# Performance work log

Measured on AMD Instinct MI355X. Metric: run time of the kernel, lower is better.

The kernel has to match this reference:

```python
import jax, jax.numpy as jnp
import numpy as np

B, S, D, H = 4, 2048, 512, 8
HD = D // H


def rotate_half(t):
    half = t.shape[-1] // 2
    return jnp.concatenate([-t[..., half:], t[..., :half]], axis=-1)


def setup_inputs() -> dict:
    key = jax.random.key(0)
    ks = jax.random.split(key, 8)
    x = jax.random.normal(ks[0], (B, S, D), dtype=jnp.float32)
    # realistic rotary tables built from angles
    inv_freq = 1.0 / (10000.0 ** (jnp.arange(0, D // 2, dtype=jnp.float32) / (D // 2)))
    ang = jnp.arange(S, dtype=jnp.float32)[:, None] * inv_freq[None, :]  # [S, D/2]
    ang = jnp.concatenate([ang, ang], axis=-1)  # [S, D]
    cos_emb = jnp.cos(ang)[None]  # [1, S, D]
    sin_emb = jnp.sin(ang)[None]
    mask = jax.random.randint(ks[1], (B, S, S), 0, 2).astype(jnp.bool_)
    scale = 1.0 / np.sqrt(D)
    wq = jax.random.normal(ks[2], (D, D), dtype=jnp.float32) * scale
    wk = jax.random.normal(ks[3], (D, D), dtype=jnp.float32) * scale
    wv = jax.random.normal(ks[4], (D, D), dtype=jnp.float32) * scale
    wo = jax.random.normal(ks[5], (D, D), dtype=jnp.float32) * scale
    return {"x": x, "cos_emb": cos_emb, "sin_emb": sin_emb, "mask": mask,
            "wq": wq, "wk": wk, "wv": wv, "wo": wo}


def reference(x, cos_emb, sin_emb, mask, wq, wk, wv, wo):
    bsz, seqlen, dim = x.shape
    # projections (weights stored as [in, out])
    xq = x @ wq
    xk = x @ wk
    xv = x @ wv
    # RoPE applied over full dim before head split (as in original)
    xq = xq * cos_emb + rotate_half(xq) * sin_emb
    xk = xk * cos_emb + rotate_half(xk) * sin_emb
    # split heads: [B, H, S, HD]
    xq = xq.reshape(bsz, seqlen, H, HD).transpose(0, 2, 1, 3)
    xk = xk.reshape(bsz, seqlen, H, HD).transpose(0, 2, 1, 3)
    xv = xv.reshape(bsz, seqlen, H, HD).transpose(0, 2, 1, 3)
    scores = jnp.einsum('bhqd,bhkd->bhqk', xq, xk) / jnp.sqrt(jnp.float32(HD))
    scores = scores + (~mask)[:, None].astype(scores.dtype) * (-1e9)
    scores = jax.nn.softmax(scores.astype(jnp.float32), axis=-1).astype(xq.dtype)
    scores = scores * mask[:, None].astype(scores.dtype)
    out = jnp.einsum('bhqk,bhkd->bhqd', scores, xv)
    out = out.transpose(0, 2, 1, 3).reshape(bsz, seqlen, dim)
    return out @ wo
```

## Files before the change

kernel.cpp:

```cpp
#include <hip/hip_runtime.h>
#include <hip/hip_bf16.h>

typedef __bf16 bf16x8 __attribute__((ext_vector_type(8)));
typedef float f32x4 __attribute__((ext_vector_type(4)));
typedef short short8 __attribute__((ext_vector_type(8)));

#define MFMA16(a, b, c) __builtin_amdgcn_mfma_f32_16x16x32_bf16((a), (b), (c), 0, 0, 0)

static constexpr int S = 2048;
static constexpr int D = 512;
static constexpr int HD = 64;
static constexpr int KBLK = 64;
#define QSCALE 0.18033688011112042f

typedef __attribute__((address_space(1))) const unsigned int gu32;
typedef __attribute__((address_space(3))) unsigned int lu32;

__device__ __forceinline__ void gll16(const void* g, void* l) {
  __builtin_amdgcn_global_load_lds((gu32*)g, (lu32*)l, 16, 0, 0);
}

__device__ __forceinline__ unsigned short f2b(float f) {
  return __builtin_bit_cast(unsigned short, __float2bfloat16(f));
}
__device__ __forceinline__ float b2f(unsigned short u) {
  return __builtin_bit_cast(float, (unsigned)u << 16);
}

__global__ void maskbits_kernel(const int* __restrict__ m, unsigned long long* __restrict__ bits) {
  int gid = blockIdx.x * 256 + threadIdx.x;
  int lane = threadIdx.x & 63;
  unsigned long long w = __ballot(m[gid] != 0);
  if (lane == 0) bits[gid >> 6] = w;
}

__global__ void cast_x_kernel(const float* __restrict__ x, unsigned short* __restrict__ xb) {
  int idx = blockIdx.x * 256 + threadIdx.x;
  float4 v = ((const float4*)x)[idx];
  ushort4 o;
  o.x = f2b(v.x); o.y = f2b(v.y); o.z = f2b(v.z); o.w = f2b(v.w);
  ((ushort4*)xb)[idx] = o;
}

__global__ void wtrans4_kernel(const float* __restrict__ wq, const float* __restrict__ wk,
                               const float* __restrict__ wv, const float* __restrict__ wo,
                               unsigned short* __restrict__ wqkvT, unsigned short* __restrict__ woT) {
  __shared__ float t[64][65];
  const int z = blockIdx.z;
  const float* w = (z == 0) ? wq : (z == 1) ? wk : (z == 2) ? wv : wo;
  unsigned short* dst = (z < 3) ? wqkvT + (size_t)z * 512 * 512 : woT;
  const int i0 = blockIdx.x * 64, o0 = blockIdx.y * 64;
  for (int it = 0; it < 16; ++it) {
    int idx = it * 256 + threadIdx.x;
    int ii = idx >> 6, oo = idx & 63;
    t[oo][ii] = w[(size_t)(i0 + ii) * 512 + o0 + oo];
  }
  __syncthreads();
  for (int it = 0; it < 16; ++it) {
    int idx = it * 256 + threadIdx.x;
    int oo = idx >> 6, ii = idx & 63;
    dst[(size_t)(o0 + oo) * 512 + i0 + ii] = f2b(t[oo][ii]);
  }
}

__global__ __launch_bounds__(256)
void gemm2(const unsigned short* __restrict__ A, const unsigned short* __restrict__ Bt,
           int M, int N, int K, float* __restrict__ Cf,
           unsigned short* __restrict__ qd, unsigned short* __restrict__ kd,
           unsigned short* __restrict__ vtd, int mode) {
  __shared__ alignas(16) unsigned short lds[2][2][4096];
  const int tid = threadIdx.x;
  const int lane = tid & 63, l15 = lane & 15, lg = lane >> 4;
  const int wave = tid >> 6;
  const int m0 = blockIdx.x * 128, n0 = blockIdx.y * 128;
  const int wm = (wave >> 1) * 64, wn = (wave & 1) * 64;
  const int wbase = wave * 512;
  const int grow = tid >> 2, gcol = (tid & 3) * 8;
  f32x4 acc[4][4] = {};
  const int nt = K / 32;

#define GSTAGE(sb, kk)                                                              \
  do {                                                                              \
    gll16(&A[(size_t)(m0 + grow) * K + (kk) + gcol], &lds[sb][0][wbase]);           \
    gll16(&A[(size_t)(m0 + 64 + grow) * K + (kk) + gcol], &lds[sb][0][2048 + wbase]);\
    gll16(&Bt[(size_t)(n0 + grow) * K + (kk) + gcol], &lds[sb][1][wbase]);          \
    gll16(&Bt[(size_t)(n0 + 64 + grow) * K + (kk) + gcol], &lds[sb][1][2048 + wbase]);\
  } while (0)

  GSTAGE(0, 0);
  asm volatile("s_waitcnt vmcnt(0)" ::: "memory");
  __syncthreads();
  for (int t = 0; t < nt; ++t) {
    const int cur = t & 1;
    if (t + 1 < nt) GSTAGE(cur ^ 1, (t + 1) * 32);
    bf16x8 af[4], bfr[4];
#pragma unroll
    for (int i = 0; i < 4; ++i) {
      af[i]  = *(const bf16x8*)&lds[cur][0][(wm + i * 16 + l15) * 32 + lg * 8];
      bfr[i] = *(const bf16x8*)&lds[cur][1][(wn + i * 16 + l15) * 32 + lg * 8];
    }
    __builtin_amdgcn_s_setprio(1);
#pragma unroll
    for (int i = 0; i < 4; ++i)
#pragma unroll
      for (int j = 0; j < 4; ++j)
        acc[i][j] = MFMA16(af[i], bfr[j], acc[i][j]);
    __builtin_amdgcn_s_setprio(0);
    asm volatile("s_waitcnt vmcnt(0)" ::: "memory");
    __syncthreads();
  }
#undef GSTAGE

  if (mode == 0) {
#pragma unroll
    for (int i = 0; i < 4; ++i)
#pragma unroll
      for (int j = 0; j < 4; ++j)
#pragma unroll
        for (int r = 0; r < 4; ++r)
          Cf[(size_t)(m0 + wm + i * 16 + lg * 4 + r) * N + (n0 + wn + j * 16 + l15)] = acc[i][j][r];
  } else {
    const int sel = n0 >> 9;
    const int nb = (n0 & 511) + wn;
    if (sel < 2) {
      unsigned short* dst = (sel == 0) ? qd : kd;
#pragma unroll
      for (int i = 0; i < 4; ++i)
#pragma unroll
        for (int j = 0; j < 4; ++j)
#pragma unroll
          for (int r = 0; r < 4; ++r) {
            const int m = m0 + wm + i * 16 + lg * 4 + r;
            const int nn = nb + j * 16 + l15;
            dst[(((size_t)(m >> 11) * 8 + (nn >> 6)) * 2048 + (m & 2047)) * 64 + (nn & 63)] =
                f2b(acc[i][j][r]);
          }
    } else {
#pragma unroll
      for (int i = 0; i < 4; ++i)
#pragma unroll
        for (int j = 0; j < 4; ++j)
#pragma unroll
          for (int r = 0; r < 4; ++r) {
            const int m = m0 + wm + i * 16 + lg * 4 + r;
            const int nn = nb + j * 16 + l15;
            vtd[(((size_t)(m >> 11) * 8 + (nn >> 6)) * 64 + (nn & 63)) * 2048 + (m & 2047)] =
                f2b(acc[i][j][r]);
          }
    }
  }
}

__global__ void rope_pair_kernel(const unsigned short* __restrict__ qpre, const unsigned short* __restrict__ kpre,
                                 const float* __restrict__ cose, const float* __restrict__ sine,
                                 unsigned short* __restrict__ qb, unsigned short* __restrict__ kb) {
  const int idx = blockIdx.x * 256 + threadIdx.x;
  const int hd0 = (idx & 7) * 8;
  const int rr = idx >> 3;
  const int b = rr >> 13, h = (rr >> 11) & 3, s = rr & 2047;
  const size_t lo = ((size_t)(b * 8 + h) * 2048 + s) * 64 + hd0;
  const size_t hi = lo + (size_t)4 * 2048 * 64;
  const int d0 = h * 64 + hd0;
  short8 qlo = *(const short8*)&qpre[lo];
  short8 qhi = *(const short8*)&qpre[hi];
  short8 klo = *(const short8*)&kpre[lo];
  short8 khi = *(const short8*)&kpre[hi];
  float4 c0 = *(const float4*)&cose[(size_t)s * 512 + d0];
  float4 c1 = *(const float4*)&cose[(size_t)s * 512 + d0 + 4];
  float4 s0 = *(const float4*)&sine[(size_t)s * 512 + d0];
  float4 s1 = *(const float4*)&sine[(size_t)s * 512 + d0 + 4];
  float cc[8] = {c0.x, c0.y, c0.z, c0.w, c1.x, c1.y, c1.z, c1.w};
  float ss[8] = {s0.x, s0.y, s0.z, s0.w, s1.x, s1.y, s1.z, s1.w};
  short8 qolo, qohi, kolo, kohi;
#pragma unroll
  for (int j = 0; j < 8; ++j) {
    float ql = b2f((unsigned short)qlo[j]), qh = b2f((unsigned short)qhi[j]);
    float kl = b2f((unsigned short)klo[j]), kh = b2f((unsigned short)khi[j]);
    qolo[j] = (short)f2b((ql * cc[j] - qh * ss[j]) * QSCALE);
    qohi[j] = (short)f2b((qh * cc[j] + ql * ss[j]) * QSCALE);
    kolo[j] = (short)f2b(kl * cc[j] - kh * ss[j]);
    kohi[j] = (short)f2b(kh * cc[j] + kl * ss[j]);
  }
  *(short8*)&qb[lo] = qolo;
  *(short8*)&qb[hi] = qohi;
  *(short8*)&kb[lo] = kolo;
  *(short8*)&kb[hi] = kohi;
}

__global__ __launch_bounds__(512)
void flash_kernel(const unsigned short* __restrict__ qb, const unsigned short* __restrict__ kb,
                  const unsigned short* __restrict__ vtb, const unsigned long long* __restrict__ mbits,
                  float* __restrict__ op0, float* __restrict__ op1,
                  float* __restrict__ ls0, float* __restrict__ ls1) {
  __shared__ alignas(16) unsigned short kv[3][2][4096];
  __shared__ alignas(16) f32x4 btab[16];
  const int tid = threadIdx.x;
  const int wave = tid >> 6, lane = tid & 63;
  const int l15 = lane & 15, lg = lane >> 4;
  const int swz = (l15 & 7) << 4;
  const int wgid = blockIdx.x;
  const int slot = wgid >> 3;
  const int bh = (wgid & 7) * 4 + (slot & 3);
  const int rest = slot >> 2;
  const int kh = rest & 1;
  const int q0 = (rest >> 1) * 128 + wave * 16;
  const int b = bh >> 3, h = bh & 7;
  const int kbase = kh * 1024;
  const unsigned short* Q = qb + ((size_t)bh * S + q0) * HD;
  const unsigned short* Kp = kb + (size_t)bh * S * HD;
  const unsigned short* Vt = vtb + (size_t)bh * HD * S;
  const unsigned long long* Mrow = mbits + ((size_t)b * S + q0 + l15) * (S / 64) + kh * 16;
  float* opart = kh ? op1 : op0;
  float* lsum = kh ? ls1 : ls0;

  const int srow = tid >> 3;
  const int scol = ((tid & 7) ^ (srow & 7)) * 8;
  const int ksrow = ((srow & 15) >> 2) * 8 + ((srow >> 4) & 1) * 4 + (srow & 3) + (srow >> 5) * 32;
  const int wbase = wave * 512;

  if (tid < 16) {
    f32x4 e;
    e[0] = (tid & 1) ? 0.f : -300.f;
    e[1] = (tid & 2) ? 0.f : -300.f;
    e[2] = (tid & 4) ? 0.f : -300.f;
    e[3] = (tid & 8) ? 0.f : -300.f;
    btab[tid] = e;
  }

  bf16x8 qf0 = *(const bf16x8*)&Q[l15 * HD + lg * 8];
  bf16x8 qf1 = *(const bf16x8*)&Q[l15 * HD + 32 + lg * 8];
  f32x4 o[4] = {};
  float lpart = 0.f;
  const int lgs8 = lg * 8;

  unsigned long long wA = Mrow[0];
  gll16(&Kp[(size_t)(kbase + ksrow) * HD + scol], &kv[0][0][wbase]);
  gll16(&Vt[(size_t)srow * S + kbase + scol], &kv[0][1][wbase]);
  unsigned long long wB = Mrow[1];
  gll16(&Kp[(size_t)(kbase + 64 + ksrow) * HD + scol], &kv[1][0][wbase]);
  gll16(&Vt[(size_t)srow * S + kbase + 64 + scol], &kv[1][1][wbase]);
  asm volatile("s_waitcnt vmcnt(3) lgkmcnt(0)" ::: "memory");
  __builtin_amdgcn_s_barrier();

  int bi = 0;
  for (int t = 0; t < 16; ++t) {
    unsigned long long wC = 0;
    if (t + 2 < 16) {
      const int kn = kbase + (t + 2) * KBLK;
      const int bn = (bi == 0) ? 2 : bi - 1;
      wC = Mrow[t + 2];
      gll16(&Kp[(size_t)(kn + ksrow) * HD + scol], &kv[bn][0][wbase]);
      gll16(&Vt[(size_t)srow * S + kn + scol], &kv[bn][1][wbase]);
    }
    const char* kbp = (const char*)&kv[bi][0][0];
    const char* vbp = (const char*)&kv[bi][1][0];

    f32x4 sc[4] = {};
    __builtin_amdgcn_s_setprio(1);
#pragma unroll
    for (int n = 0; n < 4; ++n) {
      const int cb = (n * 16 + l15) * 128 + ((lg * 16) ^ swz);
      bf16x8 kf0 = *(const bf16x8*)(kbp + cb);
      bf16x8 kf1 = *(const bf16x8*)(kbp + (cb ^ 64));
      sc[n] = MFMA16(kf0, qf0, sc[n]);
      sc[n] = MFMA16(kf1, qf1, sc[n]);
    }
    __builtin_amdgcn_s_setprio(0);

    f32x4 pv[4];
    {
      const unsigned nib0 = (unsigned)(wA >> (lgs8 + 0)) & 15u;
      const unsigned nib1 = (unsigned)(wA >> (lgs8 + 4)) & 15u;
      const unsigned nib2 = (unsigned)(wA >> (lgs8 + 32)) & 15u;
      const unsigned nib3 = (unsigned)(wA >> (lgs8 + 36)) & 15u;
      const f32x4 b0 = btab[nib0], b1 = btab[nib1], b2 = btab[nib2], b3 = btab[nib3];
#pragma unroll
      for (int r = 0; r < 4; ++r) {
        pv[0][r] = __builtin_amdgcn_exp2f(sc[0][r] + b0[r]);
        pv[1][r] = __builtin_amdgcn_exp2f(sc[1][r] + b1[r]);
        pv[2][r] = __builtin_amdgcn_exp2f(sc[2][r] + b2[r]);
        pv[3][r] = __builtin_amdgcn_exp2f(sc[3][r] + b3[r]);
      }
    }
    f32x4 s4 = (pv[0] + pv[1]) + (pv[2] + pv[3]);
    lpart += (s4[0] + s4[1]) + (s4[2] + s4[3]);

    bf16x8 pf0, pf1;
#pragma unroll
    for (int j = 0; j < 4; ++j) {
      pf0[j]     = (__bf16)pv[0][j];
      pf0[j + 4] = (__bf16)pv[1][j];
      pf1[j]     = (__bf16)pv[2][j];
      pf1[j + 4] = (__bf16)pv[3][j];
    }

    __builtin_amdgcn_s_setprio(1);
#pragma unroll
    for (int n = 0; n < 4; ++n) {
      const int cb = (n * 16 + l15) * 128 + ((lg * 16) ^ swz);
      bf16x8 vf0 = *(const bf16x8*)(vbp + cb);
      bf16x8 vf1 = *(const bf16x8*)(vbp + (cb ^ 64));
      o[n] = MFMA16(pf0, vf0, o[n]);
      o[n] = MFMA16(pf1, vf1, o[n]);
    }
    __builtin_amdgcn_s_setprio(0);

    if (t < 14) { asm volatile("s_waitcnt vmcnt(3)" ::: "memory"); }
    else        { asm volatile("s_waitcnt vmcnt(0)" ::: "memory"); }
    __builtin_amdgcn_s_barrier();
    wA = wB; wB = wC;
    bi = (bi == 2) ? 0 : bi + 1;
  }

  lpart += __shfl_xor(lpart, 16);
  lpart += __shfl_xor(lpart, 32);
  if (lg == 0) lsum[(size_t)bh * S + q0 + l15] = lpart;
#pragma unroll
  for (int r = 0; r < 4; ++r)
#pragma unroll
    for (int n = 0; n < 4; ++n)
      opart[((size_t)(b * S + q0 + lg * 4 + r)) * D + h * HD + n * 16 + l15] = o[n][r];
}

__global__ __launch_bounds__(256)
void gemm_fused(const float* __restrict__ op0, const float* __restrict__ op1,
                const float* __restrict__ ls0, const float* __restrict__ ls1,
                const unsigned short* __restrict__ Bt, float* __restrict__ C) {
  __shared__ alignas(16) unsigned short ldsA[2][2048];
  __shared__ alignas(16) unsigned short ldsB[2][4096];
  __shared__ float invt[512];
  const int tid = threadIdx.x;
  const int lane = tid & 63, l15 = lane & 15, lg = lane >> 4;
  const int wave = tid >> 6;
  const int m0 = blockIdx.x * 64, n0 = blockIdx.y * 128;
  const int wm = (wave >> 1) * 32, wn = (wave & 1) * 64;
  const int wbase = wave * 512;
  const int grow = tid >> 2, gcol = (tid & 3) * 8;
  const int arow = m0 + (tid >> 2);
  const size_t abase = (size_t)arow * 512 + (tid & 3) * 8;
  f32x4 acc[2][4] = {};

  for (int e = tid; e < 512; e += 256) {
    const int row = e >> 3, hh = e & 7;
    const int m = m0 + row;
    const size_t li = ((size_t)((m >> 11) * 8 + hh)) * 2048 + (m & 2047);
    const float l = ls0[li] + ls1[li];
    invt[e] = (l > 0.f) ? 1.f / l : 0.f;
  }

#define BSTAGE(sb, kk)                                                               \
  do {                                                                               \
    gll16(&Bt[(size_t)(n0 + grow) * 512 + (kk) + gcol], &ldsB[sb][wbase]);           \
    gll16(&Bt[(size_t)(n0 + 64 + grow) * 512 + (kk) + gcol], &ldsB[sb][2048 + wbase]);\
  } while (0)

  float4 a0, a1, p0, p1;
#define ALOAD(kk)                                          \
  do {                                                     \
    a0 = *(const float4*)&op0[abase + (kk)];               \
    a1 = *(const float4*)&op0[abase + (kk) + 4];           \
    p0 = *(const float4*)&op1[abase + (kk)];               \
    p1 = *(const float4*)&op1[abase + (kk) + 4];           \
  } while (0)

#define AWRITE(sb, kk)                                                       \
  do {                                                                       \
    const float inv = invt[((tid >> 2) << 3) | ((kk) >> 6)];                 \
    short8 pk;                                                               \
    pk[0] = (short)f2b((a0.x + p0.x) * inv);                                 \
    pk[1] = (short)f2b((a0.y + p0.y) * inv);                                 \
    pk[2] = (short)f2b((a0.z + p0.z) * inv);                                 \
    pk[3] = (short)f2b((a0.w + p0.w) * inv);                                 \
    pk[4] = (short)f2b((a1.x + p1.x) * inv);                                 \
    pk[5] = (short)f2b((a1.y + p1.y) * inv);                                 \
    pk[6] = (short)f2b((a1.z + p1.z) * inv);                                 \
    pk[7] = (short)f2b((a1.w + p1.w) * inv);                                 \
    *(short8*)&ldsA[sb][(tid >> 2) * 32 + (tid & 3) * 8] = pk;               \
  } while (0)

  ALOAD(0);
  BSTAGE(0, 0);
  __syncthreads();
  AWRITE(0, 0);
  __syncthreads();

  for (int t = 0; t < 16; ++t) {
    const int cur = t & 1;
    const bool have = (t + 1 < 16);
    if (have) { ALOAD((t + 1) * 32); BSTAGE(cur ^ 1, (t + 1) * 32); }
    bf16x8 af[2], bfr[4];
#pragma unroll
    for (int i = 0; i < 2; ++i)
      af[i] = *(const bf16x8*)&ldsA[cur][(wm + i * 16 + l15) * 32 + lg * 8];
#pragma unroll
    for (int j = 0; j < 4; ++j)
      bfr[j] = *(const bf16x8*)&ldsB[cur][(wn + j * 16 + l15) * 32 + lg * 8];
    __builtin_amdgcn_s_setprio(1);
#pragma unroll
    for (int i = 0; i < 2; ++i)
#pragma unroll
      for (int j = 0; j < 4; ++j)
        acc[i][j] = MFMA16(af[i], bfr[j], acc[i][j]);
    __builtin_amdgcn_s_setprio(0);
    asm volatile("s_waitcnt vmcnt(0)" ::: "memory");
    __syncthreads();
    if (have) AWRITE(cur ^ 1, (t + 1) * 32);
    __syncthreads();
  }
#undef BSTAGE
#undef ALOAD
#undef AWRITE

#pragma unroll
  for (int i = 0; i < 2; ++i)
#pragma unroll
    for (int j = 0; j < 4; ++j)
#pragma unroll
      for (int r = 0; r < 4; ++r)
        C[(size_t)(m0 + wm + i * 16 + lg * 4 + r) * 512 + (n0 + wn + j * 16 + l15)] = acc[i][j][r];
}

extern "C" void kernel_launch(void* const* d_in, const int* in_sizes, int n_in,
                              void* d_out, int out_size, void* d_ws, size_t ws_size,
                              hipStream_t stream) {
  const float* x = (const float*)d_in[0];
  const float* cose = (const float*)d_in[1];
  const float* sine = (const float*)d_in[2];
  const int* mask = (const int*)d_in[3];
  const float* wq = (const float*)d_in[4];
  const float* wk = (const float*)d_in[5];
  const float* wv = (const float*)d_in[6];
  const float* wo = (const float*)d_in[7];
  float* out = (float*)d_out;
  char* ws = (char*)d_ws;

  unsigned short* xb    = (unsigned short*)(ws);
  unsigned short* wqkvT = (unsigned short*)(ws + 8388608);
  unsigned short* woT   = (unsigned short*)(ws + 9961472);
  unsigned short* qpre  = (unsigned short*)(ws + 10485760);
  unsigned short* kpre  = (unsigned short*)(ws + 18874368);
  unsigned short* qbh   = (unsigned short*)(ws + 35651584);
  unsigned short* kbh   = (unsigned short*)(ws + 44040192);
  unsigned short* vtb   = (unsigned short*)(ws + 52428800);
  unsigned long long* mbits = (unsigned long long*)(ws + 60817408);
  float* op0 = (float*)(ws + 10485760);
  float* op1 = (float*)(ws + 62914560);
  float* ls0 = (float*)(ws + 79691776);
  float* ls1 = (float*)(ws + 79953920);

  maskbits_kernel<<<65536, 256, 0, stream>>>(mask, mbits);
  cast_x_kernel<<<4096, 256, 0, stream>>>(x, xb);
  wtrans4_kernel<<<dim3(8, 8, 4), 256, 0, stream>>>(wq, wk, wv, wo, wqkvT, woT);
  gemm2<<<dim3(64, 12), 256, 0, stream>>>(xb, wqkvT, 8192, 1536, 512, nullptr, qpre, kpre, vtb, 1);
  rope_pair_kernel<<<1024, 256, 0, stream>>>(qpre, kpre, cose, sine, qbh, kbh);
  flash_kernel<<<1024, 512, 0, stream>>>(qbh, kbh, vtb, mbits, op0, op1, ls0, ls1);
  gemm_fused<<<dim3(128, 4), 256, 0, stream>>>(op0, op1, ls0, ls1, woT, out);
}
```

Measured before the change: 131.7 us.

## Switch flash attention to 32x32 MFMA with 32-row waves and remap GEMM grids

The flash kernel now uses 32x32x16 bf16 MFMA. Each wave covers 32 query rows, the block drops to 256 threads, and the K/V LDS pipeline goes from triple to double buffering with a full wait each iteration. The mask-bit bias lookup and output writes are remapped to the 32x32 accumulator layout. Both GEMM kernels also switch to a 1D grid with grouped tile ordering (8 M-tiles per group) for better L2 reuse. The larger MFMA tiles are meant to cut LDS fragment reads per flop, at the cost of less prefetch depth and more registers per wave.

New measurement: 174.9 us. 32.8% more time.

```diff
diff --git a/kernel.cpp b/kernel.cpp
--- a/kernel.cpp
+++ b/kernel.cpp
@@ -3,9 +3,11 @@
 
 typedef __bf16 bf16x8 __attribute__((ext_vector_type(8)));
 typedef float f32x4 __attribute__((ext_vector_type(4)));
+typedef float f32x16 __attribute__((ext_vector_type(16)));
 typedef short short8 __attribute__((ext_vector_type(8)));
 
 #define MFMA16(a, b, c) __builtin_amdgcn_mfma_f32_16x16x32_bf16((a), (b), (c), 0, 0, 0)
+#define MFMA32(a, b, c) __builtin_amdgcn_mfma_f32_32x32x16_bf16((a), (b), (c), 0, 0, 0)
 
 static constexpr int S = 2048;
 static constexpr int D = 512;
@@ -67,12 +69,14 @@
 void gemm2(const unsigned short* __restrict__ A, const unsigned short* __restrict__ Bt,
            int M, int N, int K, float* __restrict__ Cf,
            unsigned short* __restrict__ qd, unsigned short* __restrict__ kd,
-           unsigned short* __restrict__ vtd, int mode) {
+           unsigned short* __restrict__ vtd, int mode, int nblk) {
   __shared__ alignas(16) unsigned short lds[2][2][4096];
   const int tid = threadIdx.x;
   const int lane = tid & 63, l15 = lane & 15, lg = lane >> 4;
   const int wave = tid >> 6;
-  const int m0 = blockIdx.x * 128, n0 = blockIdx.y * 128;
+  const int wgid = blockIdx.x;
+  const int xg = wgid & 7, tg = wgid >> 3;
+  const int m0 = ((tg / nblk) * 8 + xg) * 128, n0 = (tg % nblk) * 128;
   const int wm = (wave >> 1) * 64, wn = (wave & 1) * 64;
   const int wbase = wave * 512;
   const int grow = tid >> 2, gcol = (tid & 3) * 8;
@@ -187,35 +191,36 @@
   *(short8*)&kb[hi] = kohi;
 }
 
-__global__ __launch_bounds__(512)
+__global__ __launch_bounds__(256, 4)
 void flash_kernel(const unsigned short* __restrict__ qb, const unsigned short* __restrict__ kb,
                   const unsigned short* __restrict__ vtb, const unsigned long long* __restrict__ mbits,
                   float* __restrict__ op0, float* __restrict__ op1,
                   float* __restrict__ ls0, float* __restrict__ ls1) {
-  __shared__ alignas(16) unsigned short kv[3][2][4096];
+  __shared__ alignas(16) unsigned short kv[2][2][4096];
   __shared__ alignas(16) f32x4 btab[16];
   const int tid = threadIdx.x;
   const int wave = tid >> 6, lane = tid & 63;
-  const int l15 = lane & 15, lg = lane >> 4;
-  const int swz = (l15 & 7) << 4;
+  const int l31 = lane & 31, lh = lane >> 5;
+  const int swz7 = l31 & 7;
   const int wgid = blockIdx.x;
   const int slot = wgid >> 3;
   const int bh = (wgid & 7) * 4 + (slot & 3);
   const int rest = slot >> 2;
   const int kh = rest & 1;
-  const int q0 = (rest >> 1) * 128 + wave * 16;
+  const int q0 = (rest >> 1) * 128 + wave * 32;
   const int b = bh >> 3, h = bh & 7;
   const int kbase = kh * 1024;
   const unsigned short* Q = qb + ((size_t)bh * S + q0) * HD;
   const unsigned short* Kp = kb + (size_t)bh * S * HD;
   const unsigned short* Vt = vtb + (size_t)bh * HD * S;
-  const unsigned long long* Mrow = mbits + ((size_t)b * S + q0 + l15) * (S / 64) + kh * 16;
+  const unsigned long long* Mrow = mbits + ((size_t)b * S + q0 + l31) * (S / 64) + kh * 16;
   float* opart = kh ? op1 : op0;
   float* lsum = kh ? ls1 : ls0;
 
   const int srow = tid >> 3;
-  const int scol = ((tid & 7) ^ (srow & 7)) * 8;
-  const int ksrow = ((srow & 15) >> 2) * 8 + ((srow >> 4) & 1) * 4 + (srow & 3) + (srow >> 5) * 32;
+  const int ch = tid & 7;
+  const int scol = (ch ^ (srow & 7)) * 8;
+  const int pif = 16 * ((srow >> 4) & 1) + 8 * ((srow >> 2) & 1) + 4 * ((srow >> 3) & 1) + (srow & 3);
   const int wbase = wave * 512;
 
   if (tid < 16) {
@@ -227,99 +232,106 @@
     btab[tid] = e;
   }
 
-  bf16x8 qf0 = *(const bf16x8*)&Q[l15 * HD + lg * 8];
-  bf16x8 qf1 = *(const bf16x8*)&Q[l15 * HD + 32 + lg * 8];
-  f32x4 o[4] = {};
+  bf16x8 qf[4];
+#pragma unroll
+  for (int wp = 0; wp < 4; ++wp)
+    qf[wp] = *(const bf16x8*)&Q[l31 * HD + wp * 16 + 8 * lh];
+  f32x16 o0 = {}, o1 = {};
   float lpart = 0.f;
-  const int lgs8 = lg * 8;
+  const int mb = lh * 8;
+
+#define FSTAGE(sb, kn)                                                               \
+  do {                                                                               \
+    gll16(&Kp[(size_t)((kn) + pif) * HD + scol], &kv[sb][0][wbase]);                 \
+    gll16(&Kp[(size_t)((kn) + 32 + pif) * HD + scol], &kv[sb][0][2048 + wbase]);     \
+    gll16(&Vt[(size_t)srow * S + (kn) + scol], &kv[sb][1][wbase]);                   \
+    gll16(&Vt[(size_t)(srow + 32) * S + (kn) + scol], &kv[sb][1][2048 + wbase]);     \
+  } while (0)
 
   unsigned long long wA = Mrow[0];
-  gll16(&Kp[(size_t)(kbase + ksrow) * HD + scol], &kv[0][0][wbase]);
-  gll16(&Vt[(size_t)srow * S + kbase + scol], &kv[0][1][wbase]);
-  unsigned long long wB = Mrow[1];
-  gll16(&Kp[(size_t)(kbase + 64 + ksrow) * HD + scol], &kv[1][0][wbase]);
-  gll16(&Vt[(size_t)srow * S + kbase + 64 + scol], &kv[1][1][wbase]);
-  asm volatile("s_waitcnt vmcnt(3) lgkmcnt(0)" ::: "memory");
-  __builtin_amdgcn_s_barrier();
-
-  int bi = 0;
+  FSTAGE(0, kbase);
+  asm volatile("s_waitcnt vmcnt(0) lgkmcnt(0)" ::: "memory");
+  __syncthreads();
+
   for (int t = 0; t < 16; ++t) {
-    unsigned long long wC = 0;
-    if (t + 2 < 16) {
-      const int kn = kbase + (t + 2) * KBLK;
-      const int bn = (bi == 0) ? 2 : bi - 1;
-      wC = Mrow[t + 2];
-      gll16(&Kp[(size_t)(kn + ksrow) * HD + scol], &kv[bn][0][wbase]);
-      gll16(&Vt[(size_t)srow * S + kn + scol], &kv[bn][1][wbase]);
-    }
-    const char* kbp = (const char*)&kv[bi][0][0];
-    const char* vbp = (const char*)&kv[bi][1][0];
-
-    f32x4 sc[4] = {};
+    const int cur = t & 1;
+    unsigned long long wB = 0;
+    if (t + 1 < 16) {
+      FSTAGE(cur ^ 1, kbase + (t + 1) * KBLK);
+      wB = Mrow[t + 1];
+    }
+    const char* kbp = (const char*)&kv[cur][0][0];
+    const char* vbp = (const char*)&kv[cur][1][0];
+
+    f32x16 sc0 = {}, sc1 = {};
     __builtin_amdgcn_s_setprio(1);
 #pragma unroll
-    for (int n = 0; n < 4; ++n) {
-      const int cb = (n * 16 + l15) * 128 + ((lg * 16) ^ swz);
-      bf16x8 kf0 = *(const bf16x8*)(kbp + cb);
-      bf16x8 kf1 = *(const bf16x8*)(kbp + (cb ^ 64));
-      sc[n] = MFMA16(kf0, qf0, sc[n]);
-      sc[n] = MFMA16(kf1, qf1, sc[n]);
+    for (int wp = 0; wp < 4; ++wp) {
+      const int cs = ((2 * wp + lh) ^ swz7) * 16;
+      bf16x8 kf0 = *(const bf16x8*)(kbp + l31 * 128 + cs);
+      bf16x8 kf1 = *(const bf16x8*)(kbp + (32 + l31) * 128 + cs);
+      sc0 = MFMA32(kf0, qf[wp], sc0);
+      sc1 = MFMA32(kf1, qf[wp], sc1);
     }
     __builtin_amdgcn_s_setprio(0);
 
-    f32x4 pv[4];
-    {
-      const unsigned nib0 = (unsigned)(wA >> (lgs8 + 0)) & 15u;
-      const unsigned nib1 = (unsigned)(wA >> (lgs8 + 4)) & 15u;
-      const unsigned nib2 = (unsigned)(wA >> (lgs8 + 32)) & 15u;
-      const unsigned nib3 = (unsigned)(wA >> (lgs8 + 36)) & 15u;
-      const f32x4 b0 = btab[nib0], b1 = btab[nib1], b2 = btab[nib2], b3 = btab[nib3];
-#pragma unroll
-      for (int r = 0; r < 4; ++r) {
-        pv[0][r] = __builtin_amdgcn_exp2f(sc[0][r] + b0[r]);
-        pv[1][r] = __builtin_amdgcn_exp2f(sc[1][r] + b1[r]);
-        pv[2][r] = __builtin_amdgcn_exp2f(sc[2][r] + b2[r]);
-        pv[3][r] = __builtin_amdgcn_exp2f(sc[3][r] + b3[r]);
-      }
-    }
-    f32x4 s4 = (pv[0] + pv[1]) + (pv[2] + pv[3]);
-    lpart += (s4[0] + s4[1]) + (s4[2] + s4[3]);
-
-    bf16x8 pf0, pf1;
-#pragma unroll
-    for (int j = 0; j < 4; ++j) {
-      pf0[j]     = (__bf16)pv[0][j];
-      pf0[j + 4] = (__bf16)pv[1][j];
-      pf1[j]     = (__bf16)pv[2][j];
-      pf1[j + 4] = (__bf16)pv[3][j];
+    const f32x4 b00 = btab[(unsigned)(wA >> (mb + 0)) & 15u];
+    const f32x4 b01 = btab[(unsigned)(wA >> (mb + 4)) & 15u];
+    const f32x4 b02 = btab[(unsigned)(wA >> (mb + 16)) & 15u];
+    const f32x4 b03 = btab[(unsigned)(wA >> (mb + 20)) & 15u];
+    const f32x4 b10 = btab[(unsigned)(wA >> (mb + 32)) & 15u];
+    const f32x4 b11 = btab[(unsigned)(wA >> (mb + 36)) & 15u];
+    const f32x4 b12 = btab[(unsigned)(wA >> (mb + 48)) & 15u];
+    const f32x4 b13 = btab[(unsigned)(wA >> (mb + 52)) & 15u];
+    f32x16 pv0, pv1;
+#pragma unroll
+    for (int r = 0; r < 16; ++r) {
+      const int bi = 2 * (r >> 3) + ((r >> 2) & 1);
+      const float e0 = (bi == 0) ? b00[r & 3] : (bi == 1) ? b01[r & 3] : (bi == 2) ? b02[r & 3] : b03[r & 3];
+      const float e1 = (bi == 0) ? b10[r & 3] : (bi == 1) ? b11[r & 3] : (bi == 2) ? b12[r & 3] : b13[r & 3];
+      pv0[r] = __builtin_amdgcn_exp2f(sc0[r] + e0);
+      pv1[r] = __builtin_amdgcn_exp2f(sc1[r] + e1);
+    }
+    float rs = 0.f;
+#pragma unroll
+    for (int r = 0; r < 16; ++r) rs += pv0[r] + pv1[r];
+    lpart += rs;
+
+    bf16x8 pf[4];
+#pragma unroll
+    for (int j = 0; j < 8; ++j) {
+      const int rr = (j & 3) + 4 * (j >> 2);
+      pf[0][j] = (__bf16)pv0[rr];
+      pf[1][j] = (__bf16)pv0[rr + 8];
+      pf[2][j] = (__bf16)pv1[rr];
+      pf[3][j] = (__bf16)pv1[rr + 8];
     }
 
     __builtin_amdgcn_s_setprio(1);
 #pragma unroll
-    for (int n = 0; n < 4; ++n) {
-      const int cb = (n * 16 + l15) * 128 + ((lg * 16) ^ swz);
-      bf16x8 vf0 = *(const bf16x8*)(vbp + cb);
-      bf16x8 vf1 = *(const bf16x8*)(vbp + (cb ^ 64));
-      o[n] = MFMA16(pf0, vf0, o[n]);
-      o[n] = MFMA16(pf1, vf1, o[n]);
+    for (int w = 0; w < 4; ++w) {
+      const int cs = ((2 * w + lh) ^ swz7) * 16;
+      bf16x8 vf0 = *(const bf16x8*)(vbp + l31 * 128 + cs);
+      bf16x8 vf1 = *(const bf16x8*)(vbp + (32 + l31) * 128 + cs);
+      o0 = MFMA32(pf[w], vf0, o0);
+      o1 = MFMA32(pf[w], vf1, o1);
     }
     __builtin_amdgcn_s_setprio(0);
 
-    if (t < 14) { asm volatile("s_waitcnt vmcnt(3)" ::: "memory"); }
-    else        { asm volatile("s_waitcnt vmcnt(0)" ::: "memory"); }
-    __builtin_amdgcn_s_barrier();
-    wA = wB; wB = wC;
-    bi = (bi == 2) ? 0 : bi + 1;
-  }
-
-  lpart += __shfl_xor(lpart, 16);
+    asm volatile("s_waitcnt vmcnt(0)" ::: "memory");
+    __syncthreads();
+    wA = wB;
+  }
+#undef FSTAGE
+
   lpart += __shfl_xor(lpart, 32);
-  if (lg == 0) lsum[(size_t)bh * S + q0 + l15] = lpart;
-#pragma unroll
-  for (int r = 0; r < 4; ++r)
-#pragma unroll
-    for (int n = 0; n < 4; ++n)
-      opart[((size_t)(b * S + q0 + lg * 4 + r)) * D + h * HD + n * 16 + l15] = o[n][r];
+  if (lh == 0) lsum[(size_t)bh * S + q0 + l31] = lpart;
+#pragma unroll
+  for (int r = 0; r < 16; ++r) {
+    const size_t row = (size_t)(b * S + q0 + (r & 3) + 8 * (r >> 2) + 4 * lh) * D + h * HD;
+    opart[row + l31] = o0[r];
+    opart[row + 32 + l31] = o1[r];
+  }
 }
 
 __global__ __launch_bounds__(256)
@@ -332,12 +344,13 @@
   const int tid = threadIdx.x;
   const int lane = tid & 63, l15 = lane & 15, lg = lane >> 4;
   const int wave = tid >> 6;
-  const int m0 = blockIdx.x * 64, n0 = blockIdx.y * 128;
+  const int wgid = blockIdx.x;
+  const int xg = wgid & 7, tg = wgid >> 3;
+  const int m0 = ((tg >> 2) * 8 + xg) * 64, n0 = (tg & 3) * 128;
   const int wm = (wave >> 1) * 32, wn = (wave & 1) * 64;
   const int wbase = wave * 512;
   const int grow = tid >> 2, gcol = (tid & 3) * 8;
-  const int arow = m0 + (tid >> 2);
-  const size_t abase = (size_t)arow * 512 + (tid & 3) * 8;
+  const size_t abase = (size_t)(m0 + (tid >> 2)) * 512 + (tid & 3) * 8;
   f32x4 acc[2][4] = {};
 
   for (int e = tid; e < 512; e += 256) {
@@ -451,8 +464,8 @@
   maskbits_kernel<<<65536, 256, 0, stream>>>(mask, mbits);
   cast_x_kernel<<<4096, 256, 0, stream>>>(x, xb);
   wtrans4_kernel<<<dim3(8, 8, 4), 256, 0, stream>>>(wq, wk, wv, wo, wqkvT, woT);
-  gemm2<<<dim3(64, 12), 256, 0, stream>>>(xb, wqkvT, 8192, 1536, 512, nullptr, qpre, kpre, vtb, 1);
+  gemm2<<<768, 256, 0, stream>>>(xb, wqkvT, 8192, 1536, 512, nullptr, qpre, kpre, vtb, 1, 12);
   rope_pair_kernel<<<1024, 256, 0, stream>>>(qpre, kpre, cose, sine, qbh, kbh);
-  flash_kernel<<<1024, 512, 0, stream>>>(qbh, kbh, vtb, mbits, op0, op1, ls0, ls1);
-  gemm_fused<<<dim3(128, 4), 256, 0, stream>>>(op0, op1, ls0, ls1, woT, out);
-}
+  flash_kernel<<<1024, 256, 0, stream>>>(qbh, kbh, vtb, mbits, op0, op1, ls0, ls1);
+  gemm_fused<<<512, 256, 0, stream>>>(op0, op1, ls0, ls1, woT, out);
+}
```
